# Optimization experiments

Hardware: AMD Instinct MI355X
Metric: run time of the kernel (lower is better)

## Reference

```python
import jax, jax.numpy as jnp
import numpy as np

N_EMBD = 2560
N_HEAD = 32
HEAD_DIM = N_EMBD // N_HEAD  # 80
ROTARY_DIM = 32
SEQ = 2048
BSZ = 1


def _rope_tables(seq_len, rotary_dim, base=10000.0):
    inv_freq = 1.0 / (base ** (np.arange(0, rotary_dim, 2, dtype=np.float32) / rotary_dim))
    t = np.arange(seq_len, dtype=np.float32)
    freqs = np.outer(t, inv_freq)                      # [S, rd/2]
    emb = np.concatenate([freqs, freqs], axis=-1)      # [S, rd]
    return jnp.asarray(np.cos(emb)), jnp.asarray(np.sin(emb))


def setup_inputs() -> dict:
    key = jax.random.key(0)
    k1, k2, k3, k4, k5 = jax.random.split(key, 5)
    op_size = HEAD_DIM * (N_HEAD + 2 * N_HEAD)  # fused q,k,v => 3*n_embd
    hidden_states = jax.random.normal(k1, (BSZ, SEQ, N_EMBD), dtype=jnp.float32)
    Wqkv_w = jax.random.normal(k2, (op_size, N_EMBD), dtype=jnp.float32) * 0.02
    Wqkv_b = jax.random.normal(k3, (op_size,), dtype=jnp.float32) * 0.02
    out_w = jax.random.normal(k4, (N_EMBD, N_EMBD), dtype=jnp.float32) * 0.02
    out_b = jax.random.normal(k5, (N_EMBD,), dtype=jnp.float32) * 0.02
    cos, sin = _rope_tables(SEQ, ROTARY_DIM)
    return {"hidden_states": hidden_states, "Wqkv_w": Wqkv_w, "Wqkv_b": Wqkv_b,
            "out_w": out_w, "out_b": out_b, "cos": cos, "sin": sin}


def apply_partial_rotary(x, cos, sin):
    # x: [S, B, H, D]; cos/sin: [S, rd]
    rd = cos.shape[-1]
    c = cos[:, None, None, :]
    s = sin[:, None, None, :]
    x_rot = x[..., :rd]
    # NOTE: faithful to source -- rotated half is concatenated WITHOUT negation
    tmp = jnp.concatenate([x[..., rd // 2:rd], x[..., :rd // 2]], axis=-1)
    rotten = x_rot * c + tmp * s
    return jnp.concatenate([rotten, x[..., rd:]], axis=-1)


def reference(hidden_states, Wqkv_w, Wqkv_b, out_w, out_b, cos, sin):
    bsz, q_len, _ = hidden_states.shape
    qkv = hidden_states @ Wqkv_w.T + Wqkv_b            # [B, S, 3*E]
    q, k, v = jnp.split(qkv, 3, axis=-1)
    # [B, S, H, D] -> [S, B, H, D] for rotary
    q = q.reshape(bsz, q_len, N_HEAD, HEAD_DIM).transpose(1, 0, 2, 3)
    k = k.reshape(bsz, q_len, N_HEAD, HEAD_DIM).transpose(1, 0, 2, 3)
    v = v.reshape(bsz, q_len, N_HEAD, HEAD_DIM).transpose(0, 2, 1, 3)  # [B, H, S, D]
    cos_t, sin_t = cos[:q_len], sin[:q_len]
    q = apply_partial_rotary(q, cos_t, sin_t).transpose(1, 2, 0, 3)    # [B, H, S, D]
    k = apply_partial_rotary(k, cos_t, sin_t).transpose(1, 2, 0, 3)    # [B, H, S, D]
    scale = 1.0 / jnp.sqrt(jnp.asarray(HEAD_DIM, dtype=q.dtype))
    scores = jnp.einsum('bhqd,bhkd->bhqk', q, k) * scale
    causal = jnp.tril(jnp.ones((q_len, q_len), dtype=bool))
    scores = jnp.where(causal, scores, jnp.asarray(-1e30, dtype=scores.dtype))
    probs = jax.nn.softmax(scores, axis=-1)
    out = jnp.einsum('bhqk,bhkd->bhqd', probs, v)       # [B, H, S, D]
    out = out.transpose(0, 2, 1, 3).reshape(bsz, q_len, N_EMBD)
    return out @ out_w.T + out_b
```

## Files before the change

### kernel.cpp

```cpp
#include <hip/hip_runtime.h>
#include <cstdint>
#include <cstddef>

typedef unsigned short bf16_t;
typedef __attribute__((ext_vector_type(8))) short bf16x8;
typedef __attribute__((ext_vector_type(4))) float f32x4;

__device__ __forceinline__ float bf2f(bf16_t b) {
  unsigned int u = ((unsigned int)b) << 16;
  return __builtin_bit_cast(float, u);
}
__device__ __forceinline__ bf16_t f2bf(float f) {
  unsigned int u = __builtin_bit_cast(unsigned int, f);
  u += 0x7fffu + ((u >> 16) & 1u);
  return (bf16_t)(u >> 16);
}
__device__ __forceinline__ float exp2_hw(float x) {
  return __builtin_amdgcn_exp2f(x);
}

constexpr int SEQ = 2048, NE = 2560, NH = 32, HD = 80, OP = 7680;

__global__ void cvt3(const float* __restrict__ s0, const float* __restrict__ s1,
                     const float* __restrict__ s2, bf16_t* __restrict__ d0,
                     bf16_t* __restrict__ d1, bf16_t* __restrict__ d2)
{
  constexpr int N0 = SEQ * NE / 4, N1 = OP * NE / 4;
  int t = blockIdx.x * 256 + threadIdx.x;
  const float* s; bf16_t* d;
  if (t < N0)            { s = s0; d = d0; }
  else if (t < N0 + N1)  { s = s1; d = d1; t -= N0; }
  else                   { s = s2; d = d2; t -= N0 + N1; }
  float4 v = ((const float4*)s)[t];
  ushort4 o;
  o.x = f2bf(v.x); o.y = f2bf(v.y); o.z = f2bf(v.z); o.w = f2bf(v.w);
  ((ushort4*)d)[t] = o;
}

__device__ __forceinline__ void store_out(bf16_t* p, float v) { *p = f2bf(v); }
__device__ __forceinline__ void store_out(float* p, float v)  { *p = v; }

__global__ __launch_bounds__(512, 2) void gemm256_bt_bias(
    const bf16_t* __restrict__ A,
    const bf16_t* __restrict__ B,
    const float*  __restrict__ bias,
    bf16_t* __restrict__ C,
    int M, int N, int K)
{
  __shared__ bf16_t As[2][256 * 64];
  __shared__ bf16_t Bs[2][256 * 64];

  const int tid  = threadIdx.x;
  const int lane = tid & 63;
  const int wave = tid >> 6;
  const int wm   = wave >> 2;
  const int wn   = wave & 3;
  const int lm   = lane & 15;
  const int quad = lane >> 4;
  const int m0 = blockIdx.y * 256;
  const int n0 = blockIdx.x * 256;
  const int NT = K / 64;

  const int srow = lane >> 3;
  const int scol = ((lane & 7) ^ srow) * 8;

  auto stage = [&](const bf16_t* __restrict__ P, int R0, int K0, int H, bf16_t* DST) {
#pragma unroll
    for (int cc = 0; cc < 2; ++cc) {
      const int seg = wave * 2 + cc;
      const bf16_t* src = P + (size_t)(R0 + H * 128 + seg * 8 + srow) * K + K0 + scol;
      __builtin_amdgcn_global_load_lds(
          (const __attribute__((address_space(1))) unsigned int*)src,
          (__attribute__((address_space(3))) unsigned int*)(DST + H * 8192 + seg * 512),
          16, 0, 0);
    }
  };

  const int xk0 = ((0 + quad) ^ (lm & 7)) * 8;
  const int xk1 = ((4 + quad) ^ (lm & 7)) * 8;

  const int AOFF = (wm * 128 + lm) * 64;
  const int BOFF = (wn * 64  + lm) * 64;

  f32x4 acc[8][4];
#pragma unroll
  for (int i = 0; i < 8; ++i)
#pragma unroll
    for (int j = 0; j < 4; ++j)
      acc[i][j] = (f32x4){0.f, 0.f, 0.f, 0.f};

  stage(A, m0, 0, 0, As[0]);  stage(A, m0, 0, 1, As[0]);
  stage(B, n0, 0, 0, Bs[0]);  stage(B, n0, 0, 1, Bs[0]);
  stage(A, m0, 64, 0, As[1]); stage(A, m0, 64, 1, As[1]);
  stage(B, n0, 64, 0, Bs[1]); stage(B, n0, 64, 1, Bs[1]);

  asm volatile("s_waitcnt vmcnt(8)" ::: "memory");
  __builtin_amdgcn_s_barrier();
  __builtin_amdgcn_sched_barrier(0);

  bf16x8 a[4][2], b01[2][2], b23[2][2];
#pragma unroll
  for (int j = 0; j < 2; ++j) {
    b01[j][0] = *(const bf16x8*)(&Bs[0][BOFF + j * 1024 + xk0]);
    b01[j][1] = *(const bf16x8*)(&Bs[0][BOFF + j * 1024 + xk1]);
  }
#pragma unroll
  for (int i = 0; i < 4; ++i) {
    a[i][0] = *(const bf16x8*)(&As[0][AOFF + i * 1024 + xk0]);
    a[i][1] = *(const bf16x8*)(&As[0][AOFF + i * 1024 + xk1]);
  }
  __builtin_amdgcn_sched_barrier(0);

  for (int t = 0; t < NT; ++t) {
    const int c = t & 1;
    const bf16_t* Ac = &As[c][0];
    const bf16_t* Bc = &Bs[c][0];
    const bf16_t* An = &As[c ^ 1][0];
    const bf16_t* Bn = &Bs[c ^ 1][0];

    __builtin_amdgcn_s_setprio(1);
#pragma unroll
    for (int kk = 0; kk < 2; ++kk)
#pragma unroll
      for (int i = 0; i < 2; ++i)
#pragma unroll
        for (int j = 0; j < 2; ++j)
          acc[i][j] = __builtin_amdgcn_mfma_f32_16x16x32_bf16(a[i][kk], b01[j][kk], acc[i][j], 0, 0, 0);
    __builtin_amdgcn_s_setprio(0);
#pragma unroll
    for (int j = 0; j < 2; ++j) {
      b23[j][0] = *(const bf16x8*)(Bc + BOFF + (2 + j) * 1024 + xk0);
      b23[j][1] = *(const bf16x8*)(Bc + BOFF + (2 + j) * 1024 + xk1);
    }
    __builtin_amdgcn_sched_barrier(0);
    __builtin_amdgcn_s_setprio(1);
#pragma unroll
    for (int kk = 0; kk < 2; ++kk)
#pragma unroll
      for (int i = 2; i < 4; ++i)
#pragma unroll
        for (int j = 0; j < 2; ++j)
          acc[i][j] = __builtin_amdgcn_mfma_f32_16x16x32_bf16(a[i][kk], b01[j][kk], acc[i][j], 0, 0, 0);
    __builtin_amdgcn_s_setprio(0);
    __builtin_amdgcn_sched_barrier(0);

    __builtin_amdgcn_s_setprio(1);
#pragma unroll
    for (int kk = 0; kk < 2; ++kk)
#pragma unroll
      for (int i = 0; i < 4; ++i)
#pragma unroll
        for (int j = 0; j < 2; ++j)
          acc[i][2 + j] = __builtin_amdgcn_mfma_f32_16x16x32_bf16(a[i][kk], b23[j][kk], acc[i][2 + j], 0, 0, 0);
    __builtin_amdgcn_s_setprio(0);
#pragma unroll
    for (int i = 0; i < 4; ++i) {
      a[i][0] = *(const bf16x8*)(Ac + AOFF + 4096 + i * 1024 + xk0);
      a[i][1] = *(const bf16x8*)(Ac + AOFF + 4096 + i * 1024 + xk1);
    }
    __builtin_amdgcn_sched_barrier(0);

    __builtin_amdgcn_s_setprio(1);
#pragma unroll
    for (int kk = 0; kk < 2; ++kk)
#pragma unroll
      for (int i = 0; i < 4; ++i)
#pragma unroll
        for (int j = 0; j < 2; ++j)
          acc[4 + i][j] = __builtin_amdgcn_mfma_f32_16x16x32_bf16(a[i][kk], b01[j][kk], acc[4 + i][j], 0, 0, 0);
    __builtin_amdgcn_s_setprio(0);
    __builtin_amdgcn_sched_barrier(0);

    asm volatile("s_waitcnt lgkmcnt(0)" ::: "memory");
    asm volatile("s_waitcnt vmcnt(0)"  ::: "memory");
    __builtin_amdgcn_s_barrier();
    __builtin_amdgcn_sched_barrier(0);
    if (t + 1 < NT) {
#pragma unroll
      for (int j = 0; j < 2; ++j) {
        b01[j][0] = *(const bf16x8*)(Bn + BOFF + j * 1024 + xk0);
        b01[j][1] = *(const bf16x8*)(Bn + BOFF + j * 1024 + xk1);
      }
    }
    __builtin_amdgcn_sched_barrier(0);

    __builtin_amdgcn_s_setprio(1);
#pragma unroll
    for (int kk = 0; kk < 2; ++kk)
#pragma unroll
      for (int i = 0; i < 4; ++i)
#pragma unroll
        for (int j = 0; j < 2; ++j)
          acc[4 + i][2 + j] = __builtin_amdgcn_mfma_f32_16x16x32_bf16(a[i][kk], b23[j][kk], acc[4 + i][2 + j], 0, 0, 0);
    __builtin_amdgcn_s_setprio(0);
    if (t + 2 < NT) {
      stage(B, n0, (t + 2) * 64, 0, (bf16_t*)Bs[c]);
      stage(B, n0, (t + 2) * 64, 1, (bf16_t*)Bs[c]);
      stage(A, m0, (t + 2) * 64, 0, (bf16_t*)As[c]);
      stage(A, m0, (t + 2) * 64, 1, (bf16_t*)As[c]);
    }
    if (t + 1 < NT) {
#pragma unroll
      for (int i = 0; i < 4; ++i) {
        a[i][0] = *(const bf16x8*)(An + AOFF + i * 1024 + xk0);
        a[i][1] = *(const bf16x8*)(An + AOFF + i * 1024 + xk1);
      }
    }
    __builtin_amdgcn_sched_barrier(0);
  }

#pragma unroll
  for (int i = 0; i < 8; ++i) {
#pragma unroll
    for (int j = 0; j < 4; ++j) {
      const int n = n0 + wn * 64 + j * 16 + lm;
      const float bv = bias ? bias[n] : 0.f;
#pragma unroll
      for (int r = 0; r < 4; ++r) {
        const int m = m0 + wm * 128 + i * 16 + quad * 4 + r;
        C[(size_t)m * N + n] = f2bf(acc[i][j][r] + bv);
      }
    }
  }
}

template <typename OutT>
__global__ __launch_bounds__(256, 2) void gemm_bt_bias(
    const bf16_t* __restrict__ A,
    const bf16_t* __restrict__ B,
    const float*  __restrict__ bias,
    OutT* __restrict__ C,
    int M, int N, int K, int klen)
{
  __shared__ bf16_t As[2][128 * 32];
  __shared__ bf16_t Bs[2][128 * 32];

  const int tid  = threadIdx.x;
  const int lane = tid & 63;
  const int wave = tid >> 6;
  const int m0 = blockIdx.y * 128;
  const int n0 = blockIdx.x * 128;
  const int kbeg = blockIdx.z * klen;
  OutT* Cz = C + (size_t)blockIdx.z * M * N;
  const int mw = (wave >> 1) * 64;
  const int nw = (wave & 1) * 64;
  const int lm = lane & 15;
  const int lq = lane >> 4;

  f32x4 acc[4][4];
#pragma unroll
  for (int i = 0; i < 4; ++i)
#pragma unroll
    for (int j = 0; j < 4; ++j)
      acc[i][j] = (f32x4){0.f, 0.f, 0.f, 0.f};

  const int ldr = lane >> 2;
  const int ldc = (lane & 3) * 8;

  for (int kt = kbeg; kt < kbeg + klen; kt += 64) {
#pragma unroll
    for (int sub = 0; sub < 2; ++sub) {
#pragma unroll
      for (int r = 0; r < 2; ++r) {
        const int seg = wave * 2 + r;
        const int row = seg * 16 + ldr;
        const int col = kt + sub * 32 + ldc;
        const bf16_t* ga = A + (size_t)(m0 + row) * K + col;
        const bf16_t* gb = B + (size_t)(n0 + row) * K + col;
        __builtin_amdgcn_global_load_lds(
            (const __attribute__((address_space(1))) unsigned int*)ga,
            (__attribute__((address_space(3))) unsigned int*)&As[sub][seg * 512], 16, 0, 0);
        __builtin_amdgcn_global_load_lds(
            (const __attribute__((address_space(1))) unsigned int*)gb,
            (__attribute__((address_space(3))) unsigned int*)&Bs[sub][seg * 512], 16, 0, 0);
      }
    }
    __syncthreads();

#pragma unroll
    for (int sub = 0; sub < 2; ++sub) {
      bf16x8 af[4], bfq[4];
#pragma unroll
      for (int i = 0; i < 4; ++i)
        af[i] = *(const bf16x8*)&As[sub][(mw + i * 16 + lm) * 32 + lq * 8];
#pragma unroll
      for (int j = 0; j < 4; ++j)
        bfq[j] = *(const bf16x8*)&Bs[sub][(nw + j * 16 + lm) * 32 + lq * 8];

#pragma unroll
      for (int i = 0; i < 4; ++i)
#pragma unroll
        for (int j = 0; j < 4; ++j)
          acc[i][j] = __builtin_amdgcn_mfma_f32_16x16x32_bf16(af[i], bfq[j], acc[i][j], 0, 0, 0);
    }

    __syncthreads();
  }

#pragma unroll
  for (int i = 0; i < 4; ++i) {
#pragma unroll
    for (int j = 0; j < 4; ++j) {
      const int n = n0 + nw + j * 16 + lm;
      const float bv = bias ? bias[n] : 0.f;
#pragma unroll
      for (int r = 0; r < 4; ++r) {
        const int m = m0 + mw + i * 16 + lq * 4 + r;
        store_out(&Cz[(size_t)m * N + n], acc[i][j][r] + bv);
      }
    }
  }
}

__global__ void reduce2_bias(const float* __restrict__ p, const float* __restrict__ bias,
                             float* __restrict__ out)
{
  const int t = blockIdx.x * 256 + threadIdx.x;
  const float4 a = ((const float4*)p)[t];
  const float4 b = ((const float4*)(p + (size_t)SEQ * NE))[t];
  const float4 bv = ((const float4*)bias)[t % (NE / 4)];
  float4 r;
  r.x = a.x + b.x + bv.x; r.y = a.y + b.y + bv.y;
  r.z = a.z + b.z + bv.z; r.w = a.w + b.w + bv.w;
  ((float4*)out)[t] = r;
}

constexpr int TSTR = 82;
__global__ void rope_vtrans(bf16_t* __restrict__ qkv,
                            const float* __restrict__ cosb,
                            const float* __restrict__ sinb,
                            bf16_t* __restrict__ vtg)
{
  __shared__ bf16_t T[64 * TSTR];
  const int tid = threadIdx.x;

  if (blockIdx.x < 8192) {
    const int t = blockIdx.x * 256 + tid;
    const int i  = t & 15;
    const int qk = (t >> 4) & 1;
    const int h  = (t >> 5) & 31;
    const int s  = t >> 10;
    const size_t base = (size_t)s * OP + qk * NE + h * HD;
    const float xi = bf2f(qkv[base + i]);
    const float xj = bf2f(qkv[base + i + 16]);
    const float c1 = cosb[s * 32 + i];
    const float s1 = sinb[s * 32 + i];
    const float c2 = cosb[s * 32 + i + 16];
    const float s2 = sinb[s * 32 + i + 16];
    qkv[base + i]      = f2bf(xi * c1 + xj * s1);
    qkv[base + i + 16] = f2bf(xj * c2 + xi * s2);
    return;
  }

  const int vb = blockIdx.x - 8192;
  const int h  = vb >> 5;
  const int sb = (vb & 31) * 64;
  const int voff = 2 * NE + h * HD;

#pragma unroll
  for (int i = 0; i < 10; ++i) {
    const int u = i * 256 + tid;
    const int row = u / 40, c = u % 40;
    const unsigned int w = *(const unsigned int*)(qkv + (size_t)(sb + row) * OP + voff + 2 * c);
    *(unsigned int*)&T[row * TSTR + 2 * c] = w;
  }
  __syncthreads();

  bf16_t* vh = vtg + (size_t)h * HD * SEQ;
#pragma unroll
  for (int i = 0; i < 10; ++i) {
    const int u = i * 256 + tid;
    const int d = u >> 5, sp = u & 31;
    const unsigned int lo = T[(2 * sp) * TSTR + d];
    const unsigned int hi = T[(2 * sp + 1) * TSTR + d];
    *(unsigned int*)(vh + (size_t)d * SEQ + sb + 2 * sp) = lo | (hi << 16);
  }
}

constexpr int KSTR = 104;
constexpr int VSTR = 72;
constexpr int PSTR = 72;

__global__ __launch_bounds__(256, 2) void attn_mfma(
    const bf16_t* __restrict__ qkv, const bf16_t* __restrict__ vtg,
    bf16_t* __restrict__ aout)
{
  __shared__ bf16_t Ks[2][13 * 512];
  __shared__ bf16_t Vt[2][12 * 512];
  __shared__ bf16_t Ps[4][16 * PSTR];

  const int id = blockIdx.x;
  const int h  = id & 31;
  const int uu = id >> 5;
  const int tid  = threadIdx.x;
  const int lane = tid & 63;
  const int wave = tid >> 6;
  const int lm   = lane & 15;
  const int quad = lane >> 4;

  const int koff = NE + h * HD;
  const bf16_t* vh = vtg + (size_t)h * HD * SEQ;
  const float EC = 0.1118033988749895f * 1.4426950408889634f;

  int kofs[4];
#pragma unroll
  for (int r = 0; r < 4; ++r) {
    const int seg = (r < 3) ? wave * 3 + r : 12;
    const int e = seg * 512 + lane * 8;
    const int row = e / KSTR, c = e % KSTR;
    kofs[r] = row * OP + (c < 80 ? c : c - 24);
  }
  int vofs[3];
#pragma unroll
  for (int r = 0; r < 3; ++r) {
    const int e = (wave * 3 + r) * 512 + lane * 8;
    int row = e / 72;
    const int c = e % 72;
    if (row >= 80) row -= 80;
    vofs[r] = row * SEQ + (c < 64 ? c : c - 16);
  }

  auto stage_tile = [&](int kb, int bsel) {
#pragma unroll
    for (int r = 0; r < 3; ++r) {
      const bf16_t* gk = qkv + (size_t)kb * OP + koff + kofs[r];
      __builtin_amdgcn_global_load_lds(
          (const __attribute__((address_space(1))) unsigned int*)gk,
          (__attribute__((address_space(3))) unsigned int*)&Ks[bsel][(wave * 3 + r) * 512],
          16, 0, 0);
      const bf16_t* gv = vh + kb + vofs[r];
      __builtin_amdgcn_global_load_lds(
          (const __attribute__((address_space(1))) unsigned int*)gv,
          (__attribute__((address_space(3))) unsigned int*)&Vt[bsel][(wave * 3 + r) * 512],
          16, 0, 0);
    }
    if (wave == 3) {
      const bf16_t* gk = qkv + (size_t)kb * OP + koff + kofs[3];
      __builtin_amdgcn_global_load_lds(
          (const __attribute__((address_space(1))) unsigned int*)gk,
          (__attribute__((address_space(3))) unsigned int*)&Ks[bsel][12 * 512],
          16, 0, 0);
    }
  };

#pragma unroll 1
  for (int pass = 0; pass < 2; ++pass) {
    const int qt = pass ? 31 - uu : uu;
    const int q0 = qt * 64;
    const int qg = q0 + 16 * wave + lm;

    bf16x8 qf[3];
    {
      const bf16_t* q_r = qkv + (size_t)qg * OP + h * HD;
#pragma unroll
      for (int ks = 0; ks < 3; ++ks) {
        const int col = ks * 32 + quad * 8;
        if (col < 80) qf[ks] = *(const bf16x8*)(q_r + col);
        else          qf[ks] = (bf16x8){0,0,0,0,0,0,0,0};
      }
    }

    f32x4 oacc[5];
#pragma unroll
    for (int mt = 0; mt < 5; ++mt) oacc[mt] = (f32x4){0.f,0.f,0.f,0.f};
    float lsum = 0.f;

    const int ntiles = qt + 1;
    stage_tile(0, 0);
    __syncthreads();

    int buf = 0;
#pragma unroll 1
    for (int t = 0; t < ntiles; ++t) {
      if (t + 1 < ntiles) stage_tile((t + 1) * 64, buf ^ 1);

      const bf16_t* Kb = &Ks[buf][0];
      const bf16_t* Vb = &Vt[buf][0];

      f32x4 sacc[4];
#pragma unroll
      for (int mt = 0; mt < 4; ++mt) sacc[mt] = (f32x4){0.f,0.f,0.f,0.f};
#pragma unroll
      for (int ks = 0; ks < 3; ++ks) {
        bf16x8 kf[4];
#pragma unroll
        for (int mt = 0; mt < 4; ++mt)
          kf[mt] = *(const bf16x8*)&Kb[(mt * 16 + lm) * KSTR + ks * 32 + quad * 8];
#pragma unroll
        for (int mt = 0; mt < 4; ++mt)
          sacc[mt] = __builtin_amdgcn_mfma_f32_16x16x32_bf16(kf[mt], qf[ks], sacc[mt], 0, 0, 0);
      }

      const int kb = t * 64;
      if (t == ntiles - 1) {
        const int keyb = kb + quad * 4;
#pragma unroll
        for (int mt = 0; mt < 4; ++mt) {
          float ps[4];
#pragma unroll
          for (int r = 0; r < 4; ++r) {
            float p = exp2_hw(sacc[mt][r] * EC);
            p = (keyb + mt * 16 + r > qg) ? 0.f : p;
            ps[r] = p;
          }
          lsum += (ps[0] + ps[1]) + (ps[2] + ps[3]);
          ushort4 pk;
          pk.x = f2bf(ps[0]); pk.y = f2bf(ps[1]); pk.z = f2bf(ps[2]); pk.w = f2bf(ps[3]);
          *(ushort4*)&Ps[wave][lm * PSTR + mt * 16 + quad * 4] = pk;
        }
      } else {
#pragma unroll
        for (int mt = 0; mt < 4; ++mt) {
          float ps[4];
#pragma unroll
          for (int r = 0; r < 4; ++r) ps[r] = exp2_hw(sacc[mt][r] * EC);
          lsum += (ps[0] + ps[1]) + (ps[2] + ps[3]);
          ushort4 pk;
          pk.x = f2bf(ps[0]); pk.y = f2bf(ps[1]); pk.z = f2bf(ps[2]); pk.w = f2bf(ps[3]);
          *(ushort4*)&Ps[wave][lm * PSTR + mt * 16 + quad * 4] = pk;
        }
      }

#pragma unroll
      for (int ks = 0; ks < 2; ++ks) {
        bf16x8 vf[5], pf;
#pragma unroll
        for (int mt = 0; mt < 5; ++mt)
          vf[mt] = *(const bf16x8*)&Vb[(mt * 16 + lm) * VSTR + ks * 32 + quad * 8];
        pf = *(const bf16x8*)&Ps[wave][lm * PSTR + ks * 32 + quad * 8];
#pragma unroll
        for (int mt = 0; mt < 5; ++mt)
          oacc[mt] = __builtin_amdgcn_mfma_f32_16x16x32_bf16(vf[mt], pf, oacc[mt], 0, 0, 0);
      }

      __syncthreads();
      buf ^= 1;
    }

    lsum += __shfl_xor(lsum, 16);
    lsum += __shfl_xor(lsum, 32);
    const float inv = 1.f / lsum;
    bf16_t* base = aout + (size_t)qg * NE + h * HD + quad * 4;
#pragma unroll
    for (int mt = 0; mt < 5; ++mt) {
      ushort4 st;
      st.x = f2bf(oacc[mt][0] * inv);
      st.y = f2bf(oacc[mt][1] * inv);
      st.z = f2bf(oacc[mt][2] * inv);
      st.w = f2bf(oacc[mt][3] * inv);
      *(ushort4*)(base + mt * 16) = st;
    }
  }
}

extern "C" void kernel_launch(void* const* d_in, const int* in_sizes, int n_in,
                              void* d_out, int out_size, void* d_ws, size_t ws_size,
                              hipStream_t stream)
{
  const float* hs   = (const float*)d_in[0];
  const float* wqkv = (const float*)d_in[1];
  const float* bqkv = (const float*)d_in[2];
  const float* wout = (const float*)d_in[3];
  const float* bout = (const float*)d_in[4];
  const float* cosb = (const float*)d_in[5];
  const float* sinb = (const float*)d_in[6];

  bf16_t* hs_bf   = (bf16_t*)d_ws;
  bf16_t* wqkv_bf = hs_bf   + (size_t)SEQ * NE;
  bf16_t* wout_bf = wqkv_bf + (size_t)OP * NE;
  bf16_t* qkv     = wout_bf + (size_t)NE * NE;
  bf16_t* aout    = qkv     + (size_t)SEQ * OP;
  float*  out     = (float*)d_out;
  bf16_t* vtg     = hs_bf;
  float*  pbuf    = (float*)d_ws;

  constexpr int CVT_T = (SEQ * NE + OP * NE + NE * NE) / 4;
  cvt3<<<CVT_T / 256, 256, 0, stream>>>(hs, wqkv, wout, hs_bf, wqkv_bf, wout_bf);

  gemm256_bt_bias<<<dim3(OP / 256, SEQ / 256), 512, 0, stream>>>(
      hs_bf, wqkv_bf, bqkv, qkv, SEQ, OP, NE);
  rope_vtrans<<<8192 + 1024, 256, 0, stream>>>(qkv, cosb, sinb, vtg);
  attn_mfma<<<512, 256, 0, stream>>>(qkv, vtg, aout);
  gemm_bt_bias<float><<<dim3(NE / 128, SEQ / 128, 2), 256, 0, stream>>>(
      aout, wout_bf, nullptr, pbuf, SEQ, NE, NE, NE / 2);
  reduce2_bias<<<(SEQ * NE / 4) / 256, 256, 0, stream>>>(pbuf, bout, out);
}
```

Baseline: 358.3 us.

## Process two 16-query subtiles per wave in attention to reuse K/V tiles

Each wave now computes scores and outputs for 32 query rows, as two 16-row halves, so each block covers 128 queries and the grid is halved. Every K and V fragment read from LDS feeds twice as many MFMAs, which cuts LDS and global traffic per unit of work. The causal mask now applies to the last two key tiles, and launch bounds drop to one block per CU. In exchange, register pressure rises, fewer waves are resident to hide latency, and more masked work is done on the diagonal.

```diff
diff --git a/kernel.cpp b/kernel.cpp
--- a/kernel.cpp
+++ b/kernel.cpp
@@ -381,13 +381,13 @@
 constexpr int VSTR = 72;
 constexpr int PSTR = 72;
 
-__global__ __launch_bounds__(256, 2) void attn_mfma(
+__global__ __launch_bounds__(256, 1) void attn_mfma(
     const bf16_t* __restrict__ qkv, const bf16_t* __restrict__ vtg,
     bf16_t* __restrict__ aout)
 {
   __shared__ bf16_t Ks[2][13 * 512];
   __shared__ bf16_t Vt[2][12 * 512];
-  __shared__ bf16_t Ps[4][16 * PSTR];
+  __shared__ bf16_t Ps[4][32 * PSTR];
 
   const int id = blockIdx.x;
   const int h  = id & 31;
@@ -445,27 +445,30 @@
 
 #pragma unroll 1
   for (int pass = 0; pass < 2; ++pass) {
-    const int qt = pass ? 31 - uu : uu;
-    const int q0 = qt * 64;
-    const int qg = q0 + 16 * wave + lm;
-
-    bf16x8 qf[3];
-    {
-      const bf16_t* q_r = qkv + (size_t)qg * OP + h * HD;
+    const int jt = pass ? 15 - uu : uu;
+    const int q0 = jt * 128;
+    const int qw = q0 + 32 * wave;
+
+    bf16x8 qf[2][3];
+#pragma unroll
+    for (int qh = 0; qh < 2; ++qh) {
+      const bf16_t* q_r = qkv + (size_t)(qw + qh * 16 + lm) * OP + h * HD;
 #pragma unroll
       for (int ks = 0; ks < 3; ++ks) {
         const int col = ks * 32 + quad * 8;
-        if (col < 80) qf[ks] = *(const bf16x8*)(q_r + col);
-        else          qf[ks] = (bf16x8){0,0,0,0,0,0,0,0};
-      }
-    }
-
-    f32x4 oacc[5];
-#pragma unroll
-    for (int mt = 0; mt < 5; ++mt) oacc[mt] = (f32x4){0.f,0.f,0.f,0.f};
-    float lsum = 0.f;
-
-    const int ntiles = qt + 1;
+        if (col < 80) qf[qh][ks] = *(const bf16x8*)(q_r + col);
+        else          qf[qh][ks] = (bf16x8){0,0,0,0,0,0,0,0};
+      }
+    }
+
+    f32x4 oacc[5][2];
+#pragma unroll
+    for (int mt = 0; mt < 5; ++mt)
+#pragma unroll
+      for (int qh = 0; qh < 2; ++qh) oacc[mt][qh] = (f32x4){0.f,0.f,0.f,0.f};
+    float lsum[2] = {0.f, 0.f};
+
+    const int ntiles = 2 * jt + 2;
     stage_tile(0, 0);
     __syncthreads();
 
@@ -477,9 +480,11 @@
       const bf16_t* Kb = &Ks[buf][0];
       const bf16_t* Vb = &Vt[buf][0];
 
-      f32x4 sacc[4];
-#pragma unroll
-      for (int mt = 0; mt < 4; ++mt) sacc[mt] = (f32x4){0.f,0.f,0.f,0.f};
+      f32x4 sacc[4][2];
+#pragma unroll
+      for (int mt = 0; mt < 4; ++mt)
+#pragma unroll
+        for (int qh = 0; qh < 2; ++qh) sacc[mt][qh] = (f32x4){0.f,0.f,0.f,0.f};
 #pragma unroll
       for (int ks = 0; ks < 3; ++ks) {
         bf16x8 kf[4];
@@ -488,67 +493,84 @@
           kf[mt] = *(const bf16x8*)&Kb[(mt * 16 + lm) * KSTR + ks * 32 + quad * 8];
 #pragma unroll
         for (int mt = 0; mt < 4; ++mt)
-          sacc[mt] = __builtin_amdgcn_mfma_f32_16x16x32_bf16(kf[mt], qf[ks], sacc[mt], 0, 0, 0);
+#pragma unroll
+          for (int qh = 0; qh < 2; ++qh)
+            sacc[mt][qh] = __builtin_amdgcn_mfma_f32_16x16x32_bf16(kf[mt], qf[qh][ks], sacc[mt][qh], 0, 0, 0);
       }
 
       const int kb = t * 64;
-      if (t == ntiles - 1) {
-        const int keyb = kb + quad * 4;
-#pragma unroll
-        for (int mt = 0; mt < 4; ++mt) {
-          float ps[4];
-#pragma unroll
-          for (int r = 0; r < 4; ++r) {
-            float p = exp2_hw(sacc[mt][r] * EC);
-            p = (keyb + mt * 16 + r > qg) ? 0.f : p;
-            ps[r] = p;
+      const int keyb = kb + quad * 4;
+      if (t + 2 >= ntiles) {
+#pragma unroll
+        for (int qh = 0; qh < 2; ++qh) {
+          const int qg = qw + qh * 16 + lm;
+#pragma unroll
+          for (int mt = 0; mt < 4; ++mt) {
+            float ps[4];
+#pragma unroll
+            for (int r = 0; r < 4; ++r) {
+              float p = exp2_hw(sacc[mt][qh][r] * EC);
+              p = (keyb + mt * 16 + r > qg) ? 0.f : p;
+              ps[r] = p;
+            }
+            lsum[qh] += (ps[0] + ps[1]) + (ps[2] + ps[3]);
+            ushort4 pk;
+            pk.x = f2bf(ps[0]); pk.y = f2bf(ps[1]); pk.z = f2bf(ps[2]); pk.w = f2bf(ps[3]);
+            *(ushort4*)&Ps[wave][(qh * 16 + lm) * PSTR + mt * 16 + quad * 4] = pk;
           }
-          lsum += (ps[0] + ps[1]) + (ps[2] + ps[3]);
-          ushort4 pk;
-          pk.x = f2bf(ps[0]); pk.y = f2bf(ps[1]); pk.z = f2bf(ps[2]); pk.w = f2bf(ps[3]);
-          *(ushort4*)&Ps[wave][lm * PSTR + mt * 16 + quad * 4] = pk;
         }
       } else {
 #pragma unroll
-        for (int mt = 0; mt < 4; ++mt) {
-          float ps[4];
-#pragma unroll
-          for (int r = 0; r < 4; ++r) ps[r] = exp2_hw(sacc[mt][r] * EC);
-          lsum += (ps[0] + ps[1]) + (ps[2] + ps[3]);
-          ushort4 pk;
-          pk.x = f2bf(ps[0]); pk.y = f2bf(ps[1]); pk.z = f2bf(ps[2]); pk.w = f2bf(ps[3]);
-          *(ushort4*)&Ps[wave][lm * PSTR + mt * 16 + quad * 4] = pk;
+        for (int qh = 0; qh < 2; ++qh) {
+#pragma unroll
+          for (int mt = 0; mt < 4; ++mt) {
+            float ps[4];
+#pragma unroll
+            for (int r = 0; r < 4; ++r) ps[r] = exp2_hw(sacc[mt][qh][r] * EC);
+            lsum[qh] += (ps[0] + ps[1]) + (ps[2] + ps[3]);
+            ushort4 pk;
+            pk.x = f2bf(ps[0]); pk.y = f2bf(ps[1]); pk.z = f2bf(ps[2]); pk.w = f2bf(ps[3]);
+            *(ushort4*)&Ps[wave][(qh * 16 + lm) * PSTR + mt * 16 + quad * 4] = pk;
+          }
         }
       }
 
 #pragma unroll
       for (int ks = 0; ks < 2; ++ks) {
-        bf16x8 vf[5], pf;
+        bf16x8 vf[5], pf[2];
 #pragma unroll
         for (int mt = 0; mt < 5; ++mt)
           vf[mt] = *(const bf16x8*)&Vb[(mt * 16 + lm) * VSTR + ks * 32 + quad * 8];
-        pf = *(const bf16x8*)&Ps[wave][lm * PSTR + ks * 32 + quad * 8];
+#pragma unroll
+        for (int qh = 0; qh < 2; ++qh)
+          pf[qh] = *(const bf16x8*)&Ps[wave][(qh * 16 + lm) * PSTR + ks * 32 + quad * 8];
 #pragma unroll
         for (int mt = 0; mt < 5; ++mt)
-          oacc[mt] = __builtin_amdgcn_mfma_f32_16x16x32_bf16(vf[mt], pf, oacc[mt], 0, 0, 0);
+#pragma unroll
+          for (int qh = 0; qh < 2; ++qh)
+            oacc[mt][qh] = __builtin_amdgcn_mfma_f32_16x16x32_bf16(vf[mt], pf[qh], oacc[mt][qh], 0, 0, 0);
       }
 
       __syncthreads();
       buf ^= 1;
     }
 
-    lsum += __shfl_xor(lsum, 16);
-    lsum += __shfl_xor(lsum, 32);
-    const float inv = 1.f / lsum;
-    bf16_t* base = aout + (size_t)qg * NE + h * HD + quad * 4;
-#pragma unroll
-    for (int mt = 0; mt < 5; ++mt) {
-      ushort4 st;
-      st.x = f2bf(oacc[mt][0] * inv);
-      st.y = f2bf(oacc[mt][1] * inv);
-      st.z = f2bf(oacc[mt][2] * inv);
-      st.w = f2bf(oacc[mt][3] * inv);
-      *(ushort4*)(base + mt * 16) = st;
+#pragma unroll
+    for (int qh = 0; qh < 2; ++qh) {
+      float l = lsum[qh];
+      l += __shfl_xor(l, 16);
+      l += __shfl_xor(l, 32);
+      const float inv = 1.f / l;
+      bf16_t* base = aout + (size_t)(qw + qh * 16 + lm) * NE + h * HD + quad * 4;
+#pragma unroll
+      for (int mt = 0; mt < 5; ++mt) {
+        ushort4 st;
+        st.x = f2bf(oacc[mt][qh][0] * inv);
+        st.y = f2bf(oacc[mt][qh][1] * inv);
+        st.z = f2bf(oacc[mt][qh][2] * inv);
+        st.w = f2bf(oacc[mt][qh][3] * inv);
+        *(ushort4*)(base + mt * 16) = st;
+      }
     }
   }
 }
@@ -580,7 +602,7 @@
   gemm256_bt_bias<<<dim3(OP / 256, SEQ / 256), 512, 0, stream>>>(
       hs_bf, wqkv_bf, bqkv, qkv, SEQ, OP, NE);
   rope_vtrans<<<8192 + 1024, 256, 0, stream>>>(qkv, cosb, sinb, vtg);
-  attn_mfma<<<512, 256, 0, stream>>>(qkv, vtg, aout);
+  attn_mfma<<<256, 256, 0, stream>>>(qkv, vtg, aout);
   gemm_bt_bias<float><<<dim3(NE / 128, SEQ / 128, 2), 256, 0, stream>>>(
       aout, wout_bf, nullptr, pbuf, SEQ, NE, NE, NE / 2);
   reduce2_bias<<<(SEQ * NE / 4) / 256, 256, 0, stream>>>(pbuf, bout, out);
```

New measurement: 367.2 us. 1.02x slower.
